# Kernel tuning notes

Hardware: AMD Instinct MI355X
Metric: run time of the kernel (lower is better)

## Reference

```python
import jax, jax.numpy as jnp
import numpy as np

KERNEL_MUL = 2.0
KERNEL_NUM = 5


def _mmd_rbf(x_src, x_tar):
    b = x_src.shape[0]
    total = jnp.concatenate([x_src, x_tar], axis=0)          # [2N, D]
    n = total.shape[0]
    # pairwise squared L2 distances via ||a||^2 + ||b||^2 - 2 a.b (same math,
    # avoids the O(n^2 * D) broadcasted intermediate of the torch code)
    sq = jnp.sum(total * total, axis=-1)                      # [2N]
    L2 = sq[:, None] + sq[None, :] - 2.0 * (total @ total.T)  # [2N, 2N]
    L2 = jnp.maximum(L2, 0.0)
    # bandwidth from .data -> no gradient flows through it
    bandwidth = jax.lax.stop_gradient(jnp.sum(L2)) / (n * n - n)
    bandwidth = bandwidth / (KERNEL_MUL ** (KERNEL_NUM // 2))
    kernels = jnp.zeros_like(L2)
    for i in range(KERNEL_NUM):
        kernels = kernels + jnp.exp(-L2 / (bandwidth * (KERNEL_MUL ** i)))
    XX = kernels[:b, :b]
    YY = kernels[b:, b:]
    XY = kernels[:b, b:]
    YX = kernels[b:, :b]
    return jnp.mean(XX + YY - XY - YX)


def setup_inputs() -> dict:
    key = jax.random.key(0)
    k1, k2 = jax.random.split(key)
    x_src = jax.random.normal(k1, (4096, 256), dtype=jnp.float32)
    x_tar = jax.random.normal(k2, (4096, 256), dtype=jnp.float32)
    return {"x_src": x_src, "x_tar": x_tar}


def reference(x_src, x_tar):
    return _mmd_rbf(x_src, x_tar)
```

## Files before the change

kernel.cpp:

```cpp
#include <hip/hip_runtime.h>

#define D      256
#define NROWS  8192
#define BHALF  4096
#define TILE   128
#define NT2    (NROWS / TILE)
#define NBLK   (NT2 * (NT2 + 1) / 2)
#define NGRID  256
#define NBINS  64

typedef __attribute__((ext_vector_type(8))) short  short8;
typedef __attribute__((ext_vector_type(4))) float  f32x4;


__device__ __forceinline__ unsigned short f2bf(float f) {
    unsigned u = __builtin_bit_cast(unsigned, f);
    unsigned r = (u + 0x7fffu + ((u >> 16) & 1u)) >> 16;
    return (unsigned short)r;
}

__device__ __forceinline__ void gload_lds16(const unsigned short* g, unsigned short* l) {
    __builtin_amdgcn_global_load_lds(
        (const __attribute__((address_space(1))) unsigned int*)g,
        (__attribute__((address_space(3))) unsigned int*)l,
        16, 0, 0);
}

__global__ __launch_bounds__(256)
void pre_kernel(const float* __restrict__ src, const float* __restrict__ tar,
                float* __restrict__ sq, float* __restrict__ colsum,
                double* __restrict__ sumsq, unsigned short* __restrict__ Tb) {
    __shared__ float cs[D];
    int t = threadIdx.x;
    cs[t] = 0.f;
    __syncthreads();

    int lane = t & 63, w = t >> 6;
    int rowBase = blockIdx.x * 32 + w * 8;

    float4 v[8];
    #pragma unroll
    for (int it = 0; it < 8; ++it) {
        int r = rowBase + it;
        const float* rowp = (r < BHALF) ? (src + (size_t)r * D)
                                        : (tar + (size_t)(r - BHALF) * D);
        v[it] = *(const float4*)(rowp + lane * 4);
    }

    float4 csum = make_float4(0.f, 0.f, 0.f, 0.f);
    float sqacc = 0.f;
    #pragma unroll
    for (int it = 0; it < 8; ++it) {
        int r = rowBase + it;
        ushort4 h;
        h.x = f2bf(v[it].x); h.y = f2bf(v[it].y);
        h.z = f2bf(v[it].z); h.w = f2bf(v[it].w);
        *(ushort4*)(Tb + (size_t)r * D + lane * 4) = h;
        csum.x += v[it].x; csum.y += v[it].y; csum.z += v[it].z; csum.w += v[it].w;
        float s = v[it].x * v[it].x + v[it].y * v[it].y +
                  v[it].z * v[it].z + v[it].w * v[it].w;
        #pragma unroll
        for (int off = 32; off; off >>= 1) s += __shfl_xor(s, off, 64);
        if (lane == 0) { sq[r] = s; sqacc += s; }
    }
    atomicAdd(&cs[lane * 4 + 0], csum.x);
    atomicAdd(&cs[lane * 4 + 1], csum.y);
    atomicAdd(&cs[lane * 4 + 2], csum.z);
    atomicAdd(&cs[lane * 4 + 3], csum.w);
    if (lane == 0) atomicAdd(sumsq, (double)sqacc);
    __syncthreads();
    atomicAdd(&colsum[t], cs[t]);
}

__global__ __launch_bounds__(256)
void mmd_main(const unsigned short* __restrict__ Tb,
              const float* __restrict__ sq, const float* __restrict__ colsum,
              const double* __restrict__ sumsq,
              double* __restrict__ bins, unsigned* __restrict__ counter,
              float* __restrict__ out)
{
    __shared__ unsigned short As[TILE * D];
    __shared__ unsigned short Bs[TILE * D];

    int t = threadIdx.x, lane = t & 63, wid = t >> 6;
    int wi = wid >> 1, wj = wid & 1;
    int lr = lane & 15, lk = lane >> 4;

    int bid = blockIdx.x;
    int sw = (bid & 7) * (NGRID / 8) + (bid >> 3);
    int pstart = (int)(((long)sw * NBLK) / NGRID);
    int pend   = (int)(((long)(sw + 1) * NBLK) / NGRID);

    int ti, tj;
    {
        int rem = pstart, a = 0;
        while (rem >= NT2 - a) { rem -= NT2 - a; ++a; }
        ti = a; tj = a + rem;
    }

    auto stageA = [&](int tt) {
        const unsigned short* g = Tb + (size_t)tt * TILE * D;
        #pragma unroll
        for (int p = 0; p < 16; ++p) {
            int q = p * 256 + t;
            int row = q >> 5, c = q & 31;
            gload_lds16(g + row * D + (((c ^ (row & 7)) << 3)), &As[q << 3]);
        }
    };
    auto stageB = [&](int tt) {
        const unsigned short* g = Tb + (size_t)tt * TILE * D;
        #pragma unroll
        for (int p = 0; p < 16; ++p) {
            int q = p * 256 + t;
            int row = q >> 5, c = q & 31;
            gload_lds16(g + row * D + (((c ^ (row & 7)) << 3)), &Bs[q << 3]);
        }
    };

    stageA(ti);
    stageB(tj);

    float4 c4 = *(const float4*)(colsum + lane * 4);
    float s = c4.x * c4.x + c4.y * c4.y + c4.z * c4.z + c4.w * c4.w;
    #pragma unroll
    for (int off = 32; off; off >>= 1) s += __shfl_xor(s, off, 64);
    double sumL2 = 2.0 * (double)NROWS * (*sumsq) - 2.0 * (double)s;
    double bwd = sumL2 / ((double)NROWS * (double)NROWS - (double)NROWS) / 4.0;
    float g2 = (float)(1.4426950408889634 / (16.0 * bwd));

    for (int p = pstart; p < pend; ++p) {
        asm volatile("s_waitcnt vmcnt(0)" ::: "memory");
        __syncthreads();

        int rowA = ti * TILE + wi * 64, rowB = tj * TILE + wj * 64;
        float sqj[4], sqi[4][4];
        #pragma unroll
        for (int n = 0; n < 4; ++n) sqj[n] = sq[rowB + n * 16 + lr];
        #pragma unroll
        for (int m = 0; m < 4; ++m)
            #pragma unroll
            for (int r = 0; r < 4; ++r)
                sqi[m][r] = sq[rowA + m * 16 + lk * 4 + r];

        f32x4 acc[4][4];
        #pragma unroll
        for (int m = 0; m < 4; ++m)
            #pragma unroll
            for (int n = 0; n < 4; ++n)
                acc[m][n] = (f32x4){0.f, 0.f, 0.f, 0.f};

        #pragma unroll
        for (int ks = 0; ks < 8; ++ks) {
            short8 a[4], b[4];
            #pragma unroll
            for (int m = 0; m < 4; ++m) {
                int rA = wi * 64 + m * 16 + lr;
                int rB = wj * 64 + m * 16 + lr;
                int ca = ks * 4 + lk;
                a[m] = *(const short8*)&As[rA * D + ((ca ^ (rA & 7)) << 3)];
                b[m] = *(const short8*)&Bs[rB * D + ((ca ^ (rB & 7)) << 3)];
            }
            #pragma unroll
            for (int m = 0; m < 4; ++m)
                #pragma unroll
                for (int n = 0; n < 4; ++n)
                    acc[m][n] = __builtin_amdgcn_mfma_f32_16x16x32_bf16(
                                    a[m], b[n], acc[m][n], 0, 0, 0);
        }
        __syncthreads();

        int nti = ti, ntj = tj;
        if (p + 1 < pend) {
            ntj = tj + 1;
            if (ntj >= NT2) { nti = ti + 1; ntj = nti; }
            stageB(ntj);
            if (nti != ti) stageA(nti);
        }

        float local = 0.f;
        #pragma unroll
        for (int m = 0; m < 4; ++m) {
            #pragma unroll
            for (int r = 0; r < 4; ++r) {
                float si = sqi[m][r];
                #pragma unroll
                for (int n = 0; n < 4; ++n) {
                    float L2 = fmaxf(si + sqj[n] - 2.f * acc[m][n][r], 0.f);
                    float u = exp2f(-L2 * g2);
                    float u2 = u * u, u4 = u2 * u2, u8 = u4 * u4, u16 = u8 * u8;
                    local += u + u2 + u4 + u8 + u16;
                }
            }
        }
        #pragma unroll
        for (int off = 32; off; off >>= 1) local += __shfl_xor(local, off, 64);
        if (lane == 0) {
            float scale = ((ti < NT2 / 2) == (tj < NT2 / 2)) ? 1.f : -1.f;
            if (ti != tj) scale *= 2.f;
            atomicAdd(&bins[((bid << 2) + wid) & (NBINS - 1)],
                      (double)(scale * local));
        }
        ti = nti; tj = ntj;
    }

    __syncthreads();
    if (t == 0) {
        __threadfence();
        unsigned old = atomicAdd(counter, 1u);
        if (old == NGRID - 1) {
            __threadfence();
            double tot = 0.0;
            for (int i = 0; i < NBINS; ++i)
                tot += ((volatile double*)bins)[i];
            out[0] = (float)(tot / ((double)BHALF * (double)BHALF));
        }
    }
}

extern "C" void kernel_launch(void* const* d_in, const int* in_sizes, int n_in,
                              void* d_out, int out_size, void* d_ws, size_t ws_size,
                              hipStream_t stream) {
    const float* src = (const float*)d_in[0];
    const float* tar = (const float*)d_in[1];
    float* out = (float*)d_out;

    char* ws = (char*)d_ws;
    double*   sumsq   = (double*)(ws + 0);
    unsigned* counter = (unsigned*)(ws + 8);
    double*   bins    = (double*)(ws + 16);
    float*    colsum  = (float*)(ws + 1024);
    float*    sq      = (float*)(ws + 4096);
    unsigned short* Tb = (unsigned short*)(ws + 36864);

    hipMemsetAsync(ws, 0, 2048, stream);
    pre_kernel<<<256, 256, 0, stream>>>(src, tar, sq, colsum, sumsq, Tb);
    mmd_main<<<NGRID, 256, 0, stream>>>(Tb, sq, colsum, sumsq, bins, counter, out);
}
```

Baseline: 133.6 us.

## Drop B-tile LDS staging, read B directly from global, double grid

The B operand tile is no longer staged in shared memory; each wave loads its B fragments straight from global memory (via L2) inside the MFMA loop, and only the A tile stays in LDS. Halving LDS use allows two blocks per CU, so the grid doubles to 512 with a launch-bounds hint of 2. The A tile is reloaded only when the row tile changes, with a blocking wait, which removes the previous prefetch overlap. Global B loads sit on the critical path of the MFMA loop and may stall on latency, and the two-block occupancy hint may force register spilling given the large accumulator set.

```diff
diff --git a/kernel.cpp b/kernel.cpp
--- a/kernel.cpp
+++ b/kernel.cpp
@@ -6,7 +6,7 @@
 #define TILE   128
 #define NT2    (NROWS / TILE)
 #define NBLK   (NT2 * (NT2 + 1) / 2)
-#define NGRID  256
+#define NGRID  512
 #define NBINS  64
 
 typedef __attribute__((ext_vector_type(8))) short  short8;
@@ -72,7 +72,7 @@
     atomicAdd(&colsum[t], cs[t]);
 }
 
-__global__ __launch_bounds__(256)
+__global__ __launch_bounds__(256, 2)
 void mmd_main(const unsigned short* __restrict__ Tb,
               const float* __restrict__ sq, const float* __restrict__ colsum,
               const double* __restrict__ sumsq,
@@ -80,7 +80,6 @@
               float* __restrict__ out)
 {
     __shared__ unsigned short As[TILE * D];
-    __shared__ unsigned short Bs[TILE * D];
 
     int t = threadIdx.x, lane = t & 63, wid = t >> 6;
     int wi = wid >> 1, wj = wid & 1;
@@ -104,21 +103,11 @@
         for (int p = 0; p < 16; ++p) {
             int q = p * 256 + t;
             int row = q >> 5, c = q & 31;
-            gload_lds16(g + row * D + (((c ^ (row & 7)) << 3)), &As[q << 3]);
+            gload_lds16(g + row * D + ((c ^ (row & 7)) << 3), &As[q << 3]);
         }
     };
-    auto stageB = [&](int tt) {
-        const unsigned short* g = Tb + (size_t)tt * TILE * D;
-        #pragma unroll
-        for (int p = 0; p < 16; ++p) {
-            int q = p * 256 + t;
-            int row = q >> 5, c = q & 31;
-            gload_lds16(g + row * D + (((c ^ (row & 7)) << 3)), &Bs[q << 3]);
-        }
-    };
 
     stageA(ti);
-    stageB(tj);
 
     float4 c4 = *(const float4*)(colsum + lane * 4);
     float s = c4.x * c4.x + c4.y * c4.y + c4.z * c4.z + c4.w * c4.w;
@@ -128,11 +117,13 @@
     double bwd = sumL2 / ((double)NROWS * (double)NROWS - (double)NROWS) / 4.0;
     float g2 = (float)(1.4426950408889634 / (16.0 * bwd));
 
+    asm volatile("s_waitcnt vmcnt(0)" ::: "memory");
+    __syncthreads();
+
     for (int p = pstart; p < pend; ++p) {
-        asm volatile("s_waitcnt vmcnt(0)" ::: "memory");
-        __syncthreads();
-
         int rowA = ti * TILE + wi * 64, rowB = tj * TILE + wj * 64;
+        const unsigned short* gB = Tb + (size_t)rowB * D;
+
         float sqj[4], sqi[4][4];
         #pragma unroll
         for (int n = 0; n < 4; ++n) sqj[n] = sq[rowB + n * 16 + lr];
@@ -152,13 +143,12 @@
         #pragma unroll
         for (int ks = 0; ks < 8; ++ks) {
             short8 a[4], b[4];
+            int ca = ks * 4 + lk;
             #pragma unroll
             for (int m = 0; m < 4; ++m) {
                 int rA = wi * 64 + m * 16 + lr;
-                int rB = wj * 64 + m * 16 + lr;
-                int ca = ks * 4 + lk;
                 a[m] = *(const short8*)&As[rA * D + ((ca ^ (rA & 7)) << 3)];
-                b[m] = *(const short8*)&Bs[rB * D + ((ca ^ (rB & 7)) << 3)];
+                b[m] = *(const short8*)(gB + (size_t)(m * 16 + lr) * D + ca * 8);
             }
             #pragma unroll
             for (int m = 0; m < 4; ++m)
@@ -166,15 +156,6 @@
                 for (int n = 0; n < 4; ++n)
                     acc[m][n] = __builtin_amdgcn_mfma_f32_16x16x32_bf16(
                                     a[m], b[n], acc[m][n], 0, 0, 0);
-        }
-        __syncthreads();
-
-        int nti = ti, ntj = tj;
-        if (p + 1 < pend) {
-            ntj = tj + 1;
-            if (ntj >= NT2) { nti = ti + 1; ntj = nti; }
-            stageB(ntj);
-            if (nti != ti) stageA(nti);
         }
 
         float local = 0.f;
@@ -197,8 +178,17 @@
         if (lane == 0) {
             float scale = ((ti < NT2 / 2) == (tj < NT2 / 2)) ? 1.f : -1.f;
             if (ti != tj) scale *= 2.f;
-            atomicAdd(&bins[((bid << 2) + wid) & (NBINS - 1)],
+            atomicAdd(&bins[((sw << 2) + wid) & (NBINS - 1)],
                       (double)(scale * local));
+        }
+
+        int nti = ti, ntj = tj + 1;
+        if (ntj >= NT2) { nti = ti + 1; ntj = nti; }
+        if (p + 1 < pend && nti != ti) {
+            __syncthreads();
+            stageA(nti);
+            asm volatile("s_waitcnt vmcnt(0)" ::: "memory");
+            __syncthreads();
         }
         ti = nti; tj = ntj;
     }
```

Result: slower. 146.5 us (+9.7%).
